# Kernel optimization log

Measured on AMD Instinct MI355X. Metric: run time of the kernel, lower is better.

Reference implementation:

```python
import jax, jax.numpy as jnp
import numpy as np
import math

N = 50000        # nodes
DEG = 16         # regular out-degree -> E = N*DEG edges, grouped by source node
B = 64           # graphs in batch
F = 128          # num_node_features
H = 128          # nhid == enhid
RATIO = 0.5      # edge_ratio
NUM_CONVS = 3
E = N * DEG


def setup_inputs() -> dict:
    key = jax.random.key(0)
    ks = jax.random.split(key, 18)
    s = 0.05
    x = jax.random.normal(ks[0], (N, F), jnp.float32)
    edge_src = jnp.repeat(jnp.arange(N, dtype=jnp.int32), DEG)          # sorted by src
    edge_dst = jax.random.randint(ks[1], (E,), 0, N, jnp.int32)
    batch = ((jnp.arange(N) * B) // N).astype(jnp.int32)                 # sorted graph ids
    edge_attr = jnp.ones((E, 1), jnp.float32)                            # edge_attr=None branch
    inp = {"x": x, "edge_attr": edge_attr, "edge_src": edge_src,
           "edge_dst": edge_dst, "batch": batch}
    # GCNConv weights: [F->H, H->H, H->H]
    inp["W_gcn0"] = jax.random.normal(ks[2], (F, H), jnp.float32) * s
    inp["b_gcn0"] = jnp.zeros((H,), jnp.float32)
    inp["W_gcn1"] = jax.random.normal(ks[3], (H, H), jnp.float32) * s
    inp["b_gcn1"] = jnp.zeros((H,), jnp.float32)
    inp["W_gcn2"] = jax.random.normal(ks[4], (H, H), jnp.float32) * s
    inp["b_gcn2"] = jnp.zeros((H,), jnp.float32)
    # EGNN edge convs: [1->H, H->H]
    inp["W_eg0"] = jax.random.normal(ks[5], (1, H), jnp.float32) * s
    inp["b_eg0"] = jnp.zeros((H,), jnp.float32)
    inp["W_eg1"] = jax.random.normal(ks[6], (H, H), jnp.float32) * s
    inp["b_eg1"] = jnp.zeros((H,), jnp.float32)
    # score convs: [H->1, H->1]
    inp["W_sc0"] = jax.random.normal(ks[7], (H, 1), jnp.float32) * s
    inp["b_sc0"] = jnp.zeros((1,), jnp.float32)
    inp["W_sc1"] = jax.random.normal(ks[8], (H, 1), jnp.float32) * s
    inp["b_sc1"] = jnp.zeros((1,), jnp.float32)
    return inp


def _gcn(x, src, dst, ew, W, b):
    # PyG GCNConv: add self-loops (weight 1), symmetric deg normalization, aggregate at dst.
    n = x.shape[0]
    loop = jnp.arange(n, dtype=src.dtype)
    src2 = jnp.concatenate([src, loop])
    dst2 = jnp.concatenate([dst, loop])
    ew2 = jnp.concatenate([ew, jnp.ones((n,), ew.dtype)])
    deg = jax.ops.segment_sum(ew2, dst2, n)
    dinv = jnp.where(deg > 0, jax.lax.rsqrt(jnp.maximum(deg, 1e-12)), 0.0)
    norm = dinv[src2] * dinv[dst2] * ew2                                  # [E+n]
    msg = (x @ W)[src2] * norm[:, None]                                    # gather + scale
    return jax.ops.segment_sum(msg, dst2, n) + b                           # scatter-add


def _egnn(e, src, W, b):
    # Edge conv: scatter edge features to their source node, gather back, linear map.
    agg = jax.ops.segment_sum(e, src, N)
    return agg[src] @ W + b


def _pool(h, batch):
    gmax = jax.ops.segment_max(h, batch, B)
    gsum = jax.ops.segment_sum(h, batch, B)
    cnt = jax.ops.segment_sum(jnp.ones((h.shape[0],), h.dtype), batch, B)
    gmean = gsum / cnt[:, None]
    return jnp.concatenate([gmax, gmean, gsum], axis=1)                    # [B, 3H]


def reference(x, edge_attr, edge_src, edge_dst, batch,
              W_gcn0, b_gcn0, W_gcn1, b_gcn1, W_gcn2, b_gcn2,
              W_eg0, b_eg0, W_eg1, b_eg1, W_sc0, b_sc0, W_sc1, b_sc1):
    gW = [W_gcn0, W_gcn1, W_gcn2]
    gb = [b_gcn0, b_gcn1, b_gcn2]
    eW = [W_eg0, W_eg1]
    eb = [b_eg0, b_eg1]
    sW = [W_sc0, W_sc1]
    sb = [b_sc0, b_sc1]
    src, dst = edge_src, edge_dst
    deg = DEG
    ew = jnp.ones((src.shape[0],), jnp.float32)
    h = x
    ea = edge_attr
    xs = jnp.zeros((B, 3 * H), jnp.float32)
    for i in range(NUM_CONVS):
        h = jax.nn.relu(_gcn(h, src, dst, ew, gW[i], gb[i]))
        if i < NUM_CONVS - 1:
            ea = jax.nn.relu(_egnn(ea, src, eW[i], eb[i]))
            score = jnp.tanh(_egnn(ea, src, sW[i], sb[i])[:, 0])           # [E_cur]
            k = math.ceil(RATIO * deg)                                      # per-src-node top-k
            vals, idx = jax.lax.top_k(score.reshape(N, deg), k)             # [N,k]
            dst = jnp.take_along_axis(dst.reshape(N, deg), idx, axis=1).reshape(-1)
            flat = (jnp.arange(N)[:, None] * deg + idx).reshape(-1)
            ea = ea[flat]
            src = jnp.repeat(jnp.arange(N, dtype=src.dtype), k)
            ew = jnp.clip(vals.reshape(-1), 0.0, 1.0)
            deg = k
        xs = xs + _pool(h, batch)
    return xs
```

## Files before the change

kernel.cpp:

```cpp
#include <hip/hip_runtime.h>
#include <math.h>

#define NNODES 50000
#define DEGREE 16
#define NGRAPH 64
#define CAP 64
#define LDB 72
#define NXCD 8
#define XRANGE (NNODES / NXCD)
#define NTILE 782
#define ACHUNK 784
#define BCAP 192
#define NFILL 2048

typedef unsigned short u16;
typedef unsigned int u32;
typedef unsigned long long u64;
using short8 = __attribute__((ext_vector_type(8))) short;
using f32x4  = __attribute__((ext_vector_type(4))) float;
using fv4    = __attribute__((ext_vector_type(4))) float;

__device__ __forceinline__ u16 f2bf(float f) {
  union { float f; u32 u; } v; v.f = f;
  u32 u = v.u;
  return (u16)((u + 0x7FFFu + ((u >> 16) & 1u)) >> 16);
}
__device__ __forceinline__ float2 bf2x2(u32 u) {
  union { u32 u; float f; } lo, hi;
  lo.u = (u & 0xFFFFu) << 16; hi.u = u & 0xFFFF0000u;
  return make_float2(lo.f, hi.f);
}
__device__ __forceinline__ u32 pack2(float x, float y) {
  return (u32)f2bf(x) | ((u32)f2bf(y) << 16);
}
__device__ __forceinline__ int lowerb(const int* b, int n, int v) {
  int lo = 0, hi = n;
  while (lo < hi) { int m = (lo + hi) >> 1; if (b[m] < v) lo = m + 1; else hi = m; }
  return lo;
}

__device__ __forceinline__ void cons8(uint4 v, float w, float* acc) {
  float2 p;
  p = bf2x2(v.x); acc[0] = fmaf(w, p.x, acc[0]); acc[1] = fmaf(w, p.y, acc[1]);
  p = bf2x2(v.y); acc[2] = fmaf(w, p.x, acc[2]); acc[3] = fmaf(w, p.y, acc[3]);
  p = bf2x2(v.z); acc[4] = fmaf(w, p.x, acc[4]); acc[5] = fmaf(w, p.y, acc[5]);
  p = bf2x2(v.w); acc[6] = fmaf(w, p.x, acc[6]); acc[7] = fmaf(w, p.y, acc[7]);
}
__device__ __forceinline__ void consP(uint4 v, float* mx, float* sm) {
  float2 p;
  p = bf2x2(v.x);
  mx[0] = fmaxf(mx[0], p.x); sm[0] += p.x; mx[1] = fmaxf(mx[1], p.y); sm[1] += p.y;
  p = bf2x2(v.y);
  mx[2] = fmaxf(mx[2], p.x); sm[2] += p.x; mx[3] = fmaxf(mx[3], p.y); sm[3] += p.y;
  p = bf2x2(v.z);
  mx[4] = fmaxf(mx[4], p.x); sm[4] += p.x; mx[5] = fmaxf(mx[5], p.y); sm[5] += p.y;
  p = bf2x2(v.w);
  mx[6] = fmaxf(mx[6], p.x); sm[6] += p.x; mx[7] = fmaxf(mx[7], p.y); sm[7] += p.y;
}

__global__ __launch_bounds__(256) void k_init(
    const float* __restrict__ eattr,
    const float* __restrict__ weg, const float* __restrict__ beg,
    const float* __restrict__ wsc, const float* __restrict__ bsc,
    const float* __restrict__ W0, const float* __restrict__ W1,
    const float* __restrict__ W2, const float* __restrict__ W3,
    float* __restrict__ ew1, float* __restrict__ agg0, u16* __restrict__ Wt,
    const int* __restrict__ edst, int* __restrict__ cnt,
    int* __restrict__ slots, int2* __restrict__ stag, int* __restrict__ scnt) {
  __shared__ int2 lbuf[NXCD * BCAP];
  __shared__ int lcnt[NXCD];
  int b = blockIdx.x, t = threadIdx.x;
  if (b < 196) {
    int i = b * 256 + t;
    if (i < NNODES) {
      const fv4* p = reinterpret_cast<const fv4*>(eattr + (size_t)i * DEGREE);
      float s = 0.f;
#pragma unroll
      for (int j = 0; j < 4; ++j) {
        fv4 w = __builtin_nontemporal_load(&p[j]);
        s += w.x + w.y + w.z + w.w;
      }
      agg0[i] = s;
      float sc = 0.f;
      for (int k = 0; k < 128; ++k) {
        float e = fmaxf(fmaf(s, weg[k], beg[k]), 0.f);
        sc = fmaf(e, wsc[k], sc);
      }
      float v1 = tanhf(fmaf(16.f, sc, bsc[0]));
      ew1[i] = fminf(fmaxf(v1, 0.f), 1.f);
    }
  } else if (b < 452) {
    int idx = (b - 196) * 256 + t;
    int which = idx >> 14, r = idx & 16383;
    int k = r >> 7, n = r & 127;
    const float* W = which == 0 ? W0 : which == 1 ? W1 : which == 2 ? W2 : W3;
    Wt[which * 16384 + n * 128 + k] = f2bf(W[k * 128 + n]);
  } else {
    int b2 = b - 452;
    if (t < NXCD) lcnt[t] = 0;
    __syncthreads();
    int e0 = b2 * ACHUNK;
    for (int k = 0; k < ACHUNK; k += 256) {
      int idx = k + t;
      int e = e0 + idx;
      if (idx < ACHUNK && e < NNODES * DEGREE) {
        int d = edst[e];
        u32 r = (u32)d / (u32)XRANGE;
        int pos = atomicAdd(&lcnt[r], 1);
        if (pos < BCAP) {
          lbuf[r * BCAP + pos] = make_int2(e, d);
        } else {
          int gp = atomicAdd(&cnt[d], 1);
          if (gp < CAP) slots[(size_t)d * CAP + gp] = e;
        }
      }
    }
    __syncthreads();
    for (int idx = t; idx < NXCD * BCAP; idx += 256) {
      int r = idx / BCAP, i = idx - r * BCAP;
      if (i < min(lcnt[r], BCAP))
        stag[((size_t)r * 1024 + b2) * BCAP + i] = lbuf[idx];
    }
    if (t < NXCD) scnt[t * 1024 + b2] = min(lcnt[t], BCAP);
  }
}

__global__ __launch_bounds__(256) void k_gemmF(
    int nFill, const int2* __restrict__ stag, const int* __restrict__ scnt,
    int* __restrict__ cnt, int* __restrict__ slots,
    int nGemm, const u16* __restrict__ A, const float* __restrict__ Af32,
    const u16* __restrict__ WtA, u16* __restrict__ outA,
    int nEg, const float* __restrict__ agg0, const float* __restrict__ weg,
    const float* __restrict__ beg, const u16* __restrict__ WtE,
    const float* __restrict__ beE, const float* __restrict__ wsc1,
    const float* __restrict__ bs1, float* __restrict__ ewOut) {
  __shared__ u16 Bs[128 * LDB];
  int b = blockIdx.x, t = threadIdx.x;
  int nWork = nGemm + nEg;
  int widx = 0, fidx = -1;
  if (nFill > 0) {
    if (b < 2 * nWork) { if (b & 1) fidx = b >> 1; else widx = b >> 1; }
    else fidx = nWork + (b - 2 * nWork);
  } else widx = b;
  if (fidx >= 0) {
    int r = fidx & (NXCD - 1), sub = fidx >> 3;
    int base[4]; int tot = 0;
#pragma unroll
    for (int q = 0; q < 4; ++q) {
      base[q] = tot;
      tot += scnt[r * 1024 + sub * 4 + q];
    }
    for (int idx = t; idx < tot; idx += 256) {
      int q = 0;
#pragma unroll
      for (int qq = 1; qq < 4; ++qq) if (idx >= base[qq]) q = qq;
      int i = idx - base[q];
      int2 v = stag[((size_t)r * 1024 + sub * 4 + q) * BCAP + i];
      int pos = atomicAdd(&cnt[v.y], 1);
      if (pos < CAP) slots[(size_t)v.y * CAP + pos] = v.x;
    }
    return;
  }
  int eg = (widx >= nGemm);
  const u16* Wsrc = eg ? WtE : WtA;
  int m0 = (eg ? (widx - nGemm) : widx) * 64;
  int wave = t >> 6, lane = t & 63;
  int lm = lane & 15, quad = lane >> 4;
  int row = m0 + wave * 16 + lm;
  short8 af[4];
  if (eg) {
    float a = (row < NNODES) ? agg0[row] : 0.f;
#pragma unroll
    for (int kc = 0; kc < 4; ++kc) {
      int k0 = kc * 32 + quad * 8;
      float v[8];
#pragma unroll
      for (int j = 0; j < 8; ++j)
        v[j] = 8.f * fmaxf(fmaf(a, weg[k0 + j], beg[k0 + j]), 0.f);
      uint4 o;
      o.x = pack2(v[0], v[1]); o.y = pack2(v[2], v[3]);
      o.z = pack2(v[4], v[5]); o.w = pack2(v[6], v[7]);
      af[kc] = *reinterpret_cast<short8*>(&o);
    }
  } else if (Af32) {
    if (row < NNODES) {
      const fv4* px = reinterpret_cast<const fv4*>(Af32 + (size_t)row * 128);
#pragma unroll
      for (int kc = 0; kc < 4; ++kc) {
        int k0 = (kc * 32 + quad * 8) >> 2;
        fv4 v0 = __builtin_nontemporal_load(&px[k0]);
        fv4 v1 = __builtin_nontemporal_load(&px[k0 + 1]);
        uint4 o;
        o.x = pack2(v0.x, v0.y); o.y = pack2(v0.z, v0.w);
        o.z = pack2(v1.x, v1.y); o.w = pack2(v1.z, v1.w);
        af[kc] = *reinterpret_cast<short8*>(&o);
      }
    } else {
      uint4 o = make_uint4(0u, 0u, 0u, 0u);
#pragma unroll
      for (int kc = 0; kc < 4; ++kc) af[kc] = *reinterpret_cast<short8*>(&o);
    }
  } else {
    if (row < NNODES) {
#pragma unroll
      for (int kc = 0; kc < 4; ++kc)
        af[kc] = *reinterpret_cast<const short8*>(
            &A[(size_t)row * 128 + kc * 32 + quad * 8]);
    } else {
      uint4 o = make_uint4(0u, 0u, 0u, 0u);
#pragma unroll
      for (int kc = 0; kc < 4; ++kc) af[kc] = *reinterpret_cast<short8*>(&o);
    }
  }
  f32x4 z = {0.f, 0.f, 0.f, 0.f};
  f32x4 acc[8];
#pragma unroll
  for (int n = 0; n < 8; ++n) acc[n] = z;
#pragma unroll
  for (int p = 0; p < 2; ++p) {
    if (p) __syncthreads();
    for (int i = t; i < 1024; i += 256) {
      int r = i >> 3, c = (i & 7) << 3;
      *reinterpret_cast<uint4*>(&Bs[r * LDB + c]) =
          *reinterpret_cast<const uint4*>(&Wsrc[r * 128 + p * 64 + c]);
    }
    __syncthreads();
#pragma unroll
    for (int kc2 = 0; kc2 < 2; ++kc2) {
      int kc = p * 2 + kc2;
#pragma unroll
      for (int n = 0; n < 8; ++n) {
        short8 bf = *reinterpret_cast<const short8*>(
            &Bs[(n * 16 + lm) * LDB + kc2 * 32 + quad * 8]);
        acc[n] = __builtin_amdgcn_mfma_f32_16x16x32_bf16(af[kc], bf, acc[n], 0, 0, 0);
      }
    }
  }
  if (!eg) {
#pragma unroll
    for (int n = 0; n < 8; ++n) {
      int col = n * 16 + lm;
#pragma unroll
      for (int r = 0; r < 4; ++r) {
        int orow = m0 + wave * 16 + quad * 4 + r;
        if (orow < NNODES) outA[(size_t)orow * 128 + col] = f2bf(acc[n][r]);
      }
    }
  } else {
    float s0 = 0.f, s1 = 0.f, s2 = 0.f, s3 = 0.f;
#pragma unroll
    for (int n = 0; n < 8; ++n) {
      int col = n * 16 + lm;
      float bb2 = beE[col], wv = wsc1[col];
      s0 = fmaf(fmaxf(acc[n][0] + bb2, 0.f), wv, s0);
      s1 = fmaf(fmaxf(acc[n][1] + bb2, 0.f), wv, s1);
      s2 = fmaf(fmaxf(acc[n][2] + bb2, 0.f), wv, s2);
      s3 = fmaf(fmaxf(acc[n][3] + bb2, 0.f), wv, s3);
    }
#pragma unroll
    for (int m = 8; m >= 1; m >>= 1) {
      s0 += __shfl_xor(s0, m, 64);
      s1 += __shfl_xor(s1, m, 64);
      s2 += __shfl_xor(s2, m, 64);
      s3 += __shfl_xor(s3, m, 64);
    }
    if (lm == 0) {
      float bsv = bs1[0];
      float sv[4] = {s0, s1, s2, s3};
#pragma unroll
      for (int r = 0; r < 4; ++r) {
        int orow = m0 + wave * 16 + quad * 4 + r;
        if (orow < NNODES) {
          float v = tanhf(fmaf(8.f, sv[r], bsv));
          ewOut[orow] = fminf(fmaxf(v, 0.f), 1.f);
        }
      }
    }
  }
}

template <int MODE>
__global__ __launch_bounds__(256) void k_agg(
    int nAgg, const u16* __restrict__ xwb, const int* __restrict__ cnt,
    const int* __restrict__ slots, const float* __restrict__ wsrc,
    const float* __restrict__ dinv, const float* __restrict__ bias,
    u16* __restrict__ hout,
    const u16* __restrict__ hpool, const int* __restrict__ batch,
    float* __restrict__ out,
    const float* __restrict__ ew1g, float* __restrict__ dv1,
    float* __restrict__ ws1,
    const float* __restrict__ ew2g, float* __restrict__ dv2,
    float* __restrict__ ws2) {
  constexpr int keep = (MODE == 0) ? 16 : (MODE == 1) ? 8 : 4;
  constexpr bool L0 = (MODE == 0);
  constexpr int poolAdd = (MODE >= 2);
  __shared__ float P[1024];
  int b = blockIdx.x, t = threadIdx.x;
  int lane = t & 63;
  int q = lane >> 4, li = lane & 15;
  if (b < nAgg) {
    int n = (b * 256 + t) >> 6;
    if (n >= NNODES) return;
    int c = min(cnt[n], CAP);
    u32 e = 0;
    if (lane < c) e = (u32)slots[(size_t)n * CAP + lane];
    if (L0) {
      u32 j = e & 15u; int srcn = (int)(e >> 4);
      float e1 = 0.f, e2 = 0.f;
      if (lane < c && j < 8u) {
        e1 = ew1g[srcn];
        if (j < 4u) e2 = ew2g[srcn];
      }
#pragma unroll
      for (int m = 32; m >= 1; m >>= 1) {
        e1 += __shfl_xor(e1, m, 64);
        e2 += __shfl_xor(e2, m, 64);
      }
      if (lane == 0) {
        float d1 = rsqrtf(1.0f + e1), d2 = rsqrtf(1.0f + e2);
        dv1[n] = d1; ws1[n] = d1 * ew1g[n];
        dv2[n] = d2; ws2[n] = d2 * ew2g[n];
      }
    }
    int kc; u32 ce;
    if (keep < 16) {
      bool valid = (lane < c) && ((e & 15u) < (u32)keep);
      u64 mask = __ballot(valid);
      kc = (int)__popcll(mask);
      u64 lt = ((u64)1 << lane) - 1;
      int pos = valid ? (int)__popcll(mask & lt) : 63 - (int)__popcll((~mask) & lt);
      ce = (u32)__builtin_amdgcn_ds_permute(pos << 2, (int)e);
    } else { kc = c; ce = e; }
    int sl = 0; float wl = 0.f;
    if (lane < kc) {
      sl = (int)(ce >> 4);
      wl = L0 ? rsqrtf(1.0f + (float)min(cnt[sl], CAP)) : wsrc[sl];
    }
    const uint4* b4 = reinterpret_cast<const uint4*>(xwb);
    uint4 selfv = b4[n * 16 + li];
    float acc[8] = {0.f, 0.f, 0.f, 0.f, 0.f, 0.f, 0.f, 0.f};
    for (int i = 0; i < kc; i += 16) {
      int r0 = i + q, r1 = i + 4 + q, r2 = i + 8 + q, r3 = i + 12 + q;
      int s0 = __shfl(sl, r0, 64); float w0 = __shfl(wl, r0, 64);
      int s1 = __shfl(sl, r1, 64); float w1 = __shfl(wl, r1, 64);
      int s2 = __shfl(sl, r2, 64); float w2 = __shfl(wl, r2, 64);
      int s3 = __shfl(sl, r3, 64); float w3 = __shfl(wl, r3, 64);
      if (r0 >= kc) { s0 = n; w0 = 0.f; }
      if (r1 >= kc) { s1 = n; w1 = 0.f; }
      if (r2 >= kc) { s2 = n; w2 = 0.f; }
      if (r3 >= kc) { s3 = n; w3 = 0.f; }
      uint4 v0 = b4[s0 * 16 + li];
      uint4 v1 = selfv, v2 = selfv, v3 = selfv;
      if (i + 4 < kc)  v1 = b4[s1 * 16 + li];
      if (i + 8 < kc)  v2 = b4[s2 * 16 + li];
      if (i + 12 < kc) v3 = b4[s3 * 16 + li];
      cons8(v0, w0, acc);
      cons8(v1, w1, acc);
      cons8(v2, w2, acc);
      cons8(v3, w3, acc);
    }
#pragma unroll
    for (int k = 0; k < 8; ++k) {
      acc[k] += __shfl_xor(acc[k], 16, 64);
      acc[k] += __shfl_xor(acc[k], 32, 64);
    }
    float di = L0 ? rsqrtf(1.0f + (float)c) : dinv[n];
    float dd = di * di;
    const f32x4* bp = reinterpret_cast<const f32x4*>(bias);
    f32x4 bv0 = bp[li * 2], bv1 = bp[li * 2 + 1];
    float2 p0 = bf2x2(selfv.x), p1 = bf2x2(selfv.y),
           p2 = bf2x2(selfv.z), p3 = bf2x2(selfv.w);
    float r0 = fmaxf(fmaf(di, acc[0], fmaf(dd, p0.x, bv0.x)), 0.f);
    float r1 = fmaxf(fmaf(di, acc[1], fmaf(dd, p0.y, bv0.y)), 0.f);
    float r2 = fmaxf(fmaf(di, acc[2], fmaf(dd, p1.x, bv0.z)), 0.f);
    float r3 = fmaxf(fmaf(di, acc[3], fmaf(dd, p1.y, bv0.w)), 0.f);
    float r4 = fmaxf(fmaf(di, acc[4], fmaf(dd, p2.x, bv1.x)), 0.f);
    float r5 = fmaxf(fmaf(di, acc[5], fmaf(dd, p2.y, bv1.y)), 0.f);
    float r6 = fmaxf(fmaf(di, acc[6], fmaf(dd, p3.x, bv1.z)), 0.f);
    float r7 = fmaxf(fmaf(di, acc[7], fmaf(dd, p3.y, bv1.w)), 0.f);
    if (q == 0) {
      uint4 o;
      o.x = pack2(r0, r1); o.y = pack2(r2, r3);
      o.z = pack2(r4, r5); o.w = pack2(r6, r7);
      reinterpret_cast<uint4*>(hout + (size_t)n * 128)[li] = o;
    }
  } else {
    int g = b - nAgg;
    int wv = t >> 6;
    int lo = lowerb(batch, NNODES, g);
    int hi = lowerb(batch, NNODES, g + 1);
    const uint4* hb4 = reinterpret_cast<const uint4*>(hpool);
    float mx[8] = {0.f, 0.f, 0.f, 0.f, 0.f, 0.f, 0.f, 0.f};
    float sm[8] = {0.f, 0.f, 0.f, 0.f, 0.f, 0.f, 0.f, 0.f};
    int n = lo + wv * 4 + q;
    for (; n + 48 < hi; n += 64) {
      uint4 v0 = hb4[(size_t)n * 16 + li];
      uint4 v1 = hb4[(size_t)(n + 16) * 16 + li];
      uint4 v2 = hb4[(size_t)(n + 32) * 16 + li];
      uint4 v3 = hb4[(size_t)(n + 48) * 16 + li];
      consP(v0, mx, sm); consP(v1, mx, sm);
      consP(v2, mx, sm); consP(v3, mx, sm);
    }
    for (; n < hi; n += 16) {
      uint4 v = hb4[(size_t)n * 16 + li];
      consP(v, mx, sm);
    }
#pragma unroll
    for (int k = 0; k < 8; ++k) {
      mx[k] = fmaxf(mx[k], __shfl_xor(mx[k], 16, 64));
      mx[k] = fmaxf(mx[k], __shfl_xor(mx[k], 32, 64));
      sm[k] += __shfl_xor(sm[k], 16, 64);
      sm[k] += __shfl_xor(sm[k], 32, 64);
    }
    if (q == 0) {
#pragma unroll
      for (int k = 0; k < 8; ++k) {
        P[(wv * 16 + li) * 16 + k] = mx[k];
        P[(wv * 16 + li) * 16 + 8 + k] = sm[k];
      }
    }
    __syncthreads();
    if (t < 128) {
      int li2 = t >> 3, k = t & 7;
      int o0 = li2 * 16 + k, o1 = o0 + 8;
      float m = fmaxf(fmaxf(P[o0], P[256 + o0]),
                      fmaxf(P[512 + o0], P[768 + o0]));
      float s = P[o1] + P[256 + o1] + P[512 + o1] + P[768 + o1];
      float cf = (float)(hi - lo);
      int col = li2 * 8 + k;
      float* og = out + g * 384;
      if (poolAdd) {
        og[col] += m; og[128 + col] += s / cf; og[256 + col] += s;
      } else {
        og[col] = m;  og[128 + col] = s / cf;  og[256 + col] = s;
      }
    }
  }
}

extern "C" void kernel_launch(void* const* d_in, const int* in_sizes, int n_in,
                              void* d_out, int out_size, void* d_ws, size_t ws_size,
                              hipStream_t stream) {
  const float* x     = (const float*)d_in[0];
  const float* eattr = (const float*)d_in[1];
  const int*   edst  = (const int*)d_in[3];
  const int*   batch = (const int*)d_in[4];
  const float* Wg0 = (const float*)d_in[5];  const float* bg0 = (const float*)d_in[6];
  const float* Wg1 = (const float*)d_in[7];  const float* bg1 = (const float*)d_in[8];
  const float* Wg2 = (const float*)d_in[9];  const float* bg2 = (const float*)d_in[10];
  const float* We0 = (const float*)d_in[11]; const float* be0 = (const float*)d_in[12];
  const float* We1 = (const float*)d_in[13]; const float* be1 = (const float*)d_in[14];
  const float* Ws0 = (const float*)d_in[15]; const float* bs0 = (const float*)d_in[16];
  const float* Ws1 = (const float*)d_in[17]; const float* bs1 = (const float*)d_in[18];
  float* out = (float*)d_out;

  char* ws = (char*)d_ws;
  const size_t NBH = (size_t)NNODES * 128 * 2;
  size_t off = 0;
  auto alloc = [&](size_t bytes) { void* p = ws + off; off = (off + bytes + 255) & ~(size_t)255; return p; };
  u16*   XWb   = (u16*)alloc(NBH);
  u16*   Hb0   = (u16*)alloc(NBH);
  u16*   Hb1   = (u16*)alloc(NBH);
  u16*   Hb2   = (u16*)alloc(NBH);
  u16*   Wtb   = (u16*)alloc(4 * 128 * 128 * 2);
  int*   slots = (int*)alloc((size_t)NNODES * CAP * 4);
  int*   cnt   = (int*)alloc((size_t)NNODES * 4);
  int2*  stag  = (int2*)alloc((size_t)NXCD * 1024 * BCAP * 8);
  int*   scnt  = (int*)alloc((size_t)NXCD * 1024 * 4);
  float* agg0  = (float*)alloc((size_t)NNODES * 4);
  float* ew1   = (float*)alloc((size_t)NNODES * 4);
  float* ew2   = (float*)alloc((size_t)NNODES * 4);
  float* dinv1 = (float*)alloc((size_t)NNODES * 4);
  float* wsrc1 = (float*)alloc((size_t)NNODES * 4);
  float* dinv2 = (float*)alloc((size_t)NNODES * 4);
  float* wsrc2 = (float*)alloc((size_t)NNODES * 4);

  hipMemsetAsync(cnt, 0, (size_t)NNODES * 4, stream);
  k_init<<<1476, 256, 0, stream>>>(eattr, We0, be0, Ws0, bs0,
                                   Wg0, Wg1, Wg2, We1, ew1, agg0, Wtb,
                                   edst, cnt, slots, stag, scnt);
  k_gemmF<<<2 * NTILE + NFILL, 256, 0, stream>>>(
      NFILL, stag, scnt, cnt, slots,
      NTILE, nullptr, x, Wtb, XWb,
      NTILE, agg0, We0, be0, Wtb + 3 * 16384, be1, Ws1, bs1, ew2);
  k_agg<0><<<12500, 256, 0, stream>>>(12500, XWb, cnt, slots, nullptr, nullptr,
                                      bg0, Hb0, nullptr, batch, nullptr,
                                      ew1, dinv1, wsrc1, ew2, dinv2, wsrc2);
  k_gemmF<<<NTILE, 256, 0, stream>>>(
      0, nullptr, nullptr, nullptr, nullptr,
      NTILE, Hb0, nullptr, Wtb + 16384, XWb,
      0, nullptr, nullptr, nullptr, nullptr, nullptr, nullptr, nullptr, nullptr);
  k_agg<1><<<12500 + NGRAPH, 256, 0, stream>>>(12500, XWb, cnt, slots, wsrc1,
                                               dinv1, bg1, Hb1, Hb0, batch, out,
                                               nullptr, nullptr, nullptr,
                                               nullptr, nullptr, nullptr);
  k_gemmF<<<NTILE, 256, 0, stream>>>(
      0, nullptr, nullptr, nullptr, nullptr,
      NTILE, Hb1, nullptr, Wtb + 2 * 16384, XWb,
      0, nullptr, nullptr, nullptr, nullptr, nullptr, nullptr, nullptr, nullptr);
  k_agg<2><<<12500 + NGRAPH, 256, 0, stream>>>(12500, XWb, cnt, slots, wsrc2,
                                               dinv2, bg2, Hb2, Hb1, batch, out,
                                               nullptr, nullptr, nullptr,
                                               nullptr, nullptr, nullptr);
  k_agg<3><<<NGRAPH, 256, 0, stream>>>(0, nullptr, cnt, slots, nullptr, nullptr,
                                       nullptr, nullptr, Hb2, batch, out,
                                       nullptr, nullptr, nullptr,
                                       nullptr, nullptr, nullptr);
}
```

Before: 297.6 us.

## Store layer-0 features in column-chunked layout for cache-local gather aggregation

```diff
diff --git a/kernel.cpp b/kernel.cpp
--- a/kernel.cpp
+++ b/kernel.cpp
@@ -12,6 +12,8 @@
 #define ACHUNK 784
 #define BCAP 192
 #define NFILL 2048
+#define CH ((size_t)NNODES * 32)
+#define NN4 ((size_t)NNODES * 4)
 
 typedef unsigned short u16;
 typedef unsigned int u32;
@@ -133,7 +135,8 @@
     int nEg, const float* __restrict__ agg0, const float* __restrict__ weg,
     const float* __restrict__ beg, const u16* __restrict__ WtE,
     const float* __restrict__ beE, const float* __restrict__ wsc1,
-    const float* __restrict__ bs1, float* __restrict__ ewOut) {
+    const float* __restrict__ bs1, float* __restrict__ ewOut,
+    int chA, int chC) {
   __shared__ u16 Bs[128 * LDB];
   int b = blockIdx.x, t = threadIdx.x;
   int nWork = nGemm + nEg;
@@ -200,6 +203,17 @@
 #pragma unroll
       for (int kc = 0; kc < 4; ++kc) af[kc] = *reinterpret_cast<short8*>(&o);
     }
+  } else if (chA) {
+    if (row < NNODES) {
+#pragma unroll
+      for (int kc = 0; kc < 4; ++kc)
+        af[kc] = *reinterpret_cast<const short8*>(
+            &A[(size_t)kc * CH + (size_t)row * 32 + quad * 8]);
+    } else {
+      uint4 o = make_uint4(0u, 0u, 0u, 0u);
+#pragma unroll
+      for (int kc = 0; kc < 4; ++kc) af[kc] = *reinterpret_cast<short8*>(&o);
+    }
   } else {
     if (row < NNODES) {
 #pragma unroll
@@ -237,13 +251,25 @@
     }
   }
   if (!eg) {
-#pragma unroll
-    for (int n = 0; n < 8; ++n) {
-      int col = n * 16 + lm;
-#pragma unroll
-      for (int r = 0; r < 4; ++r) {
-        int orow = m0 + wave * 16 + quad * 4 + r;
-        if (orow < NNODES) outA[(size_t)orow * 128 + col] = f2bf(acc[n][r]);
+    if (chC) {
+#pragma unroll
+      for (int n = 0; n < 8; ++n) {
+        size_t cb = (size_t)(n >> 1) * CH + (n & 1) * 16 + lm;
+#pragma unroll
+        for (int r = 0; r < 4; ++r) {
+          int orow = m0 + wave * 16 + quad * 4 + r;
+          if (orow < NNODES) outA[cb + (size_t)orow * 32] = f2bf(acc[n][r]);
+        }
+      }
+    } else {
+#pragma unroll
+      for (int n = 0; n < 8; ++n) {
+        int col = n * 16 + lm;
+#pragma unroll
+        for (int r = 0; r < 4; ++r) {
+          int orow = m0 + wave * 16 + quad * 4 + r;
+          if (orow < NNODES) outA[(size_t)orow * 128 + col] = f2bf(acc[n][r]);
+        }
       }
     }
   } else {
@@ -279,20 +305,72 @@
   }
 }
 
-template <int MODE>
+__global__ __launch_bounds__(256) void k_aggc(
+    const u16* __restrict__ xwb, const int* __restrict__ cnt,
+    const int* __restrict__ slots, const float* __restrict__ bias,
+    u16* __restrict__ hout,
+    const float* __restrict__ ew1g, float* __restrict__ dv1,
+    float* __restrict__ ws1,
+    const float* __restrict__ ew2g, float* __restrict__ dv2,
+    float* __restrict__ ws2) {
+  int b = blockIdx.x, t = threadIdx.x;
+  int chunk = b & 3;
+  int wave = t >> 6, lane = t & 63;
+  int n = (b >> 2) * 4 + wave;
+  int e4 = lane >> 4, c16 = lane & 15;
+  int c = min(cnt[n], CAP);
+  const u32* tb = reinterpret_cast<const u32*>(xwb) + (size_t)chunk * NNODES * 16;
+  float ax = 0.f, ay = 0.f;
+  float e1 = 0.f, e2 = 0.f;
+  for (int i = 0; i < c; i += 4) {
+    int idx = i + e4;
+    bool v = idx < c;
+    u32 ent = 0;
+    if (v) ent = (u32)slots[(size_t)n * CAP + idx];
+    int sv = v ? (int)(ent >> 4) : n;
+    float wl = v ? rsqrtf(1.f + (float)min(cnt[sv], CAP)) : 0.f;
+    if (chunk == 0) {
+      u32 j = ent & 15u;
+      if (v && c16 == 0 && j < 8u) {
+        e1 += ew1g[sv];
+        if (j < 4u) e2 += ew2g[sv];
+      }
+    }
+    float2 p = bf2x2(tb[(size_t)sv * 16 + c16]);
+    ax = fmaf(wl, p.x, ax);
+    ay = fmaf(wl, p.y, ay);
+  }
+  ax += __shfl_xor(ax, 16, 64); ax += __shfl_xor(ax, 32, 64);
+  ay += __shfl_xor(ay, 16, 64); ay += __shfl_xor(ay, 32, 64);
+  if (chunk == 0) {
+    e1 += __shfl_xor(e1, 16, 64); e1 += __shfl_xor(e1, 32, 64);
+    e2 += __shfl_xor(e2, 16, 64); e2 += __shfl_xor(e2, 32, 64);
+    if (lane == 0) {
+      float d1 = rsqrtf(1.f + e1), d2 = rsqrtf(1.f + e2);
+      dv1[n] = d1; ws1[n] = d1 * ew1g[n];
+      dv2[n] = d2; ws2[n] = d2 * ew2g[n];
+    }
+  }
+  if (e4 == 0) {
+    float di = rsqrtf(1.f + (float)c), dd = di * di;
+    float2 sf = bf2x2(tb[(size_t)n * 16 + c16]);
+    float2 bv = reinterpret_cast<const float2*>(bias)[chunk * 16 + c16];
+    float r0 = fmaxf(fmaf(di, ax, fmaf(dd, sf.x, bv.x)), 0.f);
+    float r1 = fmaxf(fmaf(di, ay, fmaf(dd, sf.y, bv.y)), 0.f);
+    reinterpret_cast<u32*>(hout)[(size_t)chunk * NNODES * 16 +
+                                 (size_t)n * 16 + c16] = pack2(r0, r1);
+  }
+}
+
+template <int MODE, int PCH>
 __global__ __launch_bounds__(256) void k_agg(
     int nAgg, const u16* __restrict__ xwb, const int* __restrict__ cnt,
     const int* __restrict__ slots, const float* __restrict__ wsrc,
     const float* __restrict__ dinv, const float* __restrict__ bias,
     u16* __restrict__ hout,
     const u16* __restrict__ hpool, const int* __restrict__ batch,
-    float* __restrict__ out,
-    const float* __restrict__ ew1g, float* __restrict__ dv1,
-    float* __restrict__ ws1,
-    const float* __restrict__ ew2g, float* __restrict__ dv2,
-    float* __restrict__ ws2) {
-  constexpr int keep = (MODE == 0) ? 16 : (MODE == 1) ? 8 : 4;
-  constexpr bool L0 = (MODE == 0);
+    float* __restrict__ out) {
+  constexpr int keep = (MODE == 1) ? 8 : 4;
   constexpr int poolAdd = (MODE >= 2);
   __shared__ float P[1024];
   int b = blockIdx.x, t = threadIdx.x;
@@ -304,37 +382,19 @@
     int c = min(cnt[n], CAP);
     u32 e = 0;
     if (lane < c) e = (u32)slots[(size_t)n * CAP + lane];
-    if (L0) {
-      u32 j = e & 15u; int srcn = (int)(e >> 4);
-      float e1 = 0.f, e2 = 0.f;
-      if (lane < c && j < 8u) {
-        e1 = ew1g[srcn];
-        if (j < 4u) e2 = ew2g[srcn];
-      }
-#pragma unroll
-      for (int m = 32; m >= 1; m >>= 1) {
-        e1 += __shfl_xor(e1, m, 64);
-        e2 += __shfl_xor(e2, m, 64);
-      }
-      if (lane == 0) {
-        float d1 = rsqrtf(1.0f + e1), d2 = rsqrtf(1.0f + e2);
-        dv1[n] = d1; ws1[n] = d1 * ew1g[n];
-        dv2[n] = d2; ws2[n] = d2 * ew2g[n];
-      }
-    }
     int kc; u32 ce;
-    if (keep < 16) {
+    {
       bool valid = (lane < c) && ((e & 15u) < (u32)keep);
       u64 mask = __ballot(valid);
       kc = (int)__popcll(mask);
       u64 lt = ((u64)1 << lane) - 1;
       int pos = valid ? (int)__popcll(mask & lt) : 63 - (int)__popcll((~mask) & lt);
       ce = (u32)__builtin_amdgcn_ds_permute(pos << 2, (int)e);
-    } else { kc = c; ce = e; }
+    }
     int sl = 0; float wl = 0.f;
     if (lane < kc) {
       sl = (int)(ce >> 4);
-      wl = L0 ? rsqrtf(1.0f + (float)min(cnt[sl], CAP)) : wsrc[sl];
+      wl = wsrc[sl];
     }
     const uint4* b4 = reinterpret_cast<const uint4*>(xwb);
     uint4 selfv = b4[n * 16 + li];
@@ -364,7 +424,7 @@
       acc[k] += __shfl_xor(acc[k], 16, 64);
       acc[k] += __shfl_xor(acc[k], 32, 64);
     }
-    float di = L0 ? rsqrtf(1.0f + (float)c) : dinv[n];
+    float di = dinv[n];
     float dd = di * di;
     const f32x4* bp = reinterpret_cast<const f32x4*>(bias);
     f32x4 bv0 = bp[li * 2], bv1 = bp[li * 2 + 1];
@@ -390,19 +450,23 @@
     int lo = lowerb(batch, NNODES, g);
     int hi = lowerb(batch, NNODES, g + 1);
     const uint4* hb4 = reinterpret_cast<const uint4*>(hpool);
+    size_t cb = PCH ? ((size_t)(li >> 2) * NN4 + (li & 3)) : 0;
+    auto rd = [&](int nn) -> uint4 {
+      return PCH ? hb4[cb + (size_t)nn * 4] : hb4[(size_t)nn * 16 + li];
+    };
     float mx[8] = {0.f, 0.f, 0.f, 0.f, 0.f, 0.f, 0.f, 0.f};
     float sm[8] = {0.f, 0.f, 0.f, 0.f, 0.f, 0.f, 0.f, 0.f};
     int n = lo + wv * 4 + q;
     for (; n + 48 < hi; n += 64) {
-      uint4 v0 = hb4[(size_t)n * 16 + li];
-      uint4 v1 = hb4[(size_t)(n + 16) * 16 + li];
-      uint4 v2 = hb4[(size_t)(n + 32) * 16 + li];
-      uint4 v3 = hb4[(size_t)(n + 48) * 16 + li];
+      uint4 v0 = rd(n);
+      uint4 v1 = rd(n + 16);
+      uint4 v2 = rd(n + 32);
+      uint4 v3 = rd(n + 48);
       consP(v0, mx, sm); consP(v1, mx, sm);
       consP(v2, mx, sm); consP(v3, mx, sm);
     }
     for (; n < hi; n += 16) {
-      uint4 v = hb4[(size_t)n * 16 + li];
+      uint4 v = rd(n);
       consP(v, mx, sm);
     }
 #pragma unroll
@@ -427,7 +491,7 @@
                       fmaxf(P[512 + o0], P[768 + o0]));
       float s = P[o1] + P[256 + o1] + P[512 + o1] + P[768 + o1];
       float cf = (float)(hi - lo);
-      int col = li2 * 8 + k;
+      int col = PCH ? ((li2 >> 2) * 32 + (li2 & 3) * 8 + k) : (li2 * 8 + k);
       float* og = out + g * 384;
       if (poolAdd) {
         og[col] += m; og[128 + col] += s / cf; og[256 + col] += s;
@@ -482,28 +546,24 @@
   k_gemmF<<<2 * NTILE + NFILL, 256, 0, stream>>>(
       NFILL, stag, scnt, cnt, slots,
       NTILE, nullptr, x, Wtb, XWb,
-      NTILE, agg0, We0, be0, Wtb + 3 * 16384, be1, Ws1, bs1, ew2);
-  k_agg<0><<<12500, 256, 0, stream>>>(12500, XWb, cnt, slots, nullptr, nullptr,
-                                      bg0, Hb0, nullptr, batch, nullptr,
-                                      ew1, dinv1, wsrc1, ew2, dinv2, wsrc2);
+      NTILE, agg0, We0, be0, Wtb + 3 * 16384, be1, Ws1, bs1, ew2,
+      0, 1);
+  k_aggc<<<50000, 256, 0, stream>>>(XWb, cnt, slots, bg0, Hb0,
+                                    ew1, dinv1, wsrc1, ew2, dinv2, wsrc2);
   k_gemmF<<<NTILE, 256, 0, stream>>>(
       0, nullptr, nullptr, nullptr, nullptr,
       NTILE, Hb0, nullptr, Wtb + 16384, XWb,
-      0, nullptr, nullptr, nullptr, nullptr, nullptr, nullptr, nullptr, nullptr);
-  k_agg<1><<<12500 + NGRAPH, 256, 0, stream>>>(12500, XWb, cnt, slots, wsrc1,
-                                               dinv1, bg1, Hb1, Hb0, batch, out,
-                                               nullptr, nullptr, nullptr,
-                                               nullptr, nullptr, nullptr);
+      0, nullptr, nullptr, nullptr, nullptr, nullptr, nullptr, nullptr, nullptr,
+      1, 0);
+  k_agg<1, 1><<<12500 + NGRAPH, 256, 0, stream>>>(12500, XWb, cnt, slots, wsrc1,
+                                                  dinv1, bg1, Hb1, Hb0, batch, out);
   k_gemmF<<<NTILE, 256, 0, stream>>>(
       0, nullptr, nullptr, nullptr, nullptr,
       NTILE, Hb1, nullptr, Wtb + 2 * 16384, XWb,
-      0, nullptr, nullptr, nullptr, nullptr, nullptr, nullptr, nullptr, nullptr);
-  k_agg<2><<<12500 + NGRAPH, 256, 0, stream>>>(12500, XWb, cnt, slots, wsrc2,
-                                               dinv2, bg2, Hb2, Hb1, batch, out,
-                                               nullptr, nullptr, nullptr,
-                                               nullptr, nullptr, nullptr);
-  k_agg<3><<<NGRAPH, 256, 0, stream>>>(0, nullptr, cnt, slots, nullptr, nullptr,
-                                       nullptr, nullptr, Hb2, batch, out,
-                                       nullptr, nullptr, nullptr,
-                                       nullptr, nullptr, nullptr);
-}
+      0, nullptr, nullptr, nullptr, nullptr, nullptr, nullptr, nullptr, nullptr,
+      0, 0);
+  k_agg<2, 0><<<12500 + NGRAPH, 256, 0, stream>>>(12500, XWb, cnt, slots, wsrc2,
+                                                  dinv2, bg2, Hb2, Hb1, batch, out);
+  k_agg<3, 0><<<NGRAPH, 256, 0, stream>>>(0, nullptr, cnt, slots, nullptr,
+                                          nullptr, nullptr, nullptr, Hb2, batch, out);
+}
```

Result: slower. 423.1 us (+42.2%).
